# Optimization experiments

Measured on AMD Instinct MI355X. Metric: run time of the kernel, lower is better.

Reference implementation:

```python
import jax, jax.numpy as jnp
import numpy as np

OLD = (32, 32)   # fine grid coord_dims
NEW = (16, 16)   # coarse grid (dims // 2)
N_ORDERS = 6     # multi-indices of total order <= 2 in 2 coords


def lin_resize(x, new_size, axis):
    # 1D linear interpolation along `axis`, align_corners=True (matches F.interpolate)
    old = x.shape[axis]
    pos = jnp.arange(new_size, dtype=x.dtype) * ((old - 1) / (new_size - 1))
    lo = jnp.clip(jnp.floor(pos).astype(jnp.int32), 0, old - 2)
    w = pos - lo.astype(x.dtype)
    xl = jnp.take(x, lo, axis=axis)
    xh = jnp.take(x, lo + 1, axis=axis)
    shp = [1] * x.ndim
    shp[axis] = new_size
    w = w.reshape(shp)
    return xl * (1.0 - w) + xh * w


def bilinear_resize(x, new_hw):
    # separable bilinear, align_corners=True; x is [..., H, W]
    x = lin_resize(x, new_hw[0], x.ndim - 2)
    return lin_resize(x, new_hw[1], x.ndim - 1)


def setup_inputs():
    key = jax.random.key(0)
    ks = jax.random.split(key, 6)
    B = 32                      # bs * n_ind_dim = 8 * 4
    G = OLD[0] * OLD[1]         # fine grid size = 1024
    m, n = 2048, 1536           # coarse constraints x coarse vars (16*16*6)
    return {
        "coeffs": jax.random.normal(ks[0], (B, G, N_ORDERS), jnp.float32),
        "rhs": jax.random.normal(ks[1], (B, G), jnp.float32),
        "steps_x": jax.random.uniform(ks[2], (B, OLD[0] - 1), jnp.float32),
        "steps_y": jax.random.uniform(ks[3], (B, OLD[1] - 1), jnp.float32),
        "A": jax.random.normal(ks[4], (B, m, n), jnp.float32) * 0.05,
        "A_rhs": jax.random.normal(ks[5], (B, m), jnp.float32),
    }


def reference(coeffs, rhs, steps_x, steps_y, A, A_rhs):
    B = coeffs.shape[0]
    new_G = NEW[0] * NEW[1]

    # --- downsample_coeffs: [B,G,O] -> [B,O,H,W] -> bilinear -> [B,newG,O]
    c = coeffs.transpose(0, 2, 1).reshape(B, N_ORDERS, OLD[0], OLD[1])
    c = bilinear_resize(c, NEW)
    new_coeffs = c.reshape(B, N_ORDERS, new_G).transpose(0, 2, 1)

    # --- downsample_rhs: [B,G] -> [B,1,H,W] -> bilinear -> [B,newG]
    r = bilinear_resize(rhs.reshape(B, 1, OLD[0], OLD[1]), NEW)
    new_rhs = r.reshape(B, new_G)

    # --- downsample_steps: drop last, pairwise sum
    nsx = steps_x[:, :-1].reshape(B, OLD[0] // 2 - 1, 2).sum(axis=-1)
    nsy = steps_y[:, :-1].reshape(B, OLD[1] // 2 - 1, 2).sum(axis=-1)

    # --- make_AtA (coarsest path: dense bmm) ---
    AtA = jnp.einsum('bmn,bmk->bnk', A, A)           # At @ A, [B,n,n]
    AtPrhs = jnp.einsum('bmn,bm->bn', A, A_rhs)      # At @ rhs
    D = jnp.sum(A * A, axis=1)                       # diag(AtA) = column sums of squares

    # --- L/U split (get_tril): L = cols <= rows, U = cols > rows ---
    n = AtA.shape[-1]
    ridx = jnp.arange(n)
    lmask = ridx[:, None] >= ridx[None, :]
    L = jnp.where(lmask, AtA, jnp.zeros((), AtA.dtype))
    U = jnp.where(lmask, jnp.zeros((), AtA.dtype), AtA)

    return (new_coeffs, new_rhs, nsx, nsy, AtA, AtPrhs, D, L, U)
```

## Files before the change

### kernel.cpp

```cpp
#include <hip/hip_runtime.h>
#include <math.h>

#define NB 32
#define M 2048
#define N 1536
#define NORD 6

#define OFF_COEFFS 0
#define OFF_RHS    49152
#define OFF_NSX    57344
#define OFF_NSY    57824
#define OFF_ATA    58304
#define OFF_ATPRHS 75555776
#define OFF_D      75604928
#define OFF_L      75654080
#define OFF_U      151151552
#define SMALL_TOTAL 58304

typedef short short8v __attribute__((ext_vector_type(8)));
typedef float f32x4 __attribute__((ext_vector_type(4)));

__device__ __forceinline__ void gload16(const void* g, void* l) {
    __builtin_amdgcn_global_load_lds(
        (const __attribute__((address_space(1))) void*)g,
        (__attribute__((address_space(3))) void*)l, 16, 0, 0);
}

__device__ __forceinline__ uint rtn_bf16(float x) {
    uint u = __float_as_uint(x);
    return (u + 0x7fffu + ((u >> 16) & 1u)) >> 16;
}

__device__ __forceinline__ void nts(float v, float* p) {
    __builtin_nontemporal_store(v, p);
}
__device__ __forceinline__ void nts4(f32x4 v, float* p) {
    __builtin_nontemporal_store(v, (f32x4*)p);
}

__global__ void small_kernel(const float* __restrict__ coeffs,
                             const float* __restrict__ rhs,
                             const float* __restrict__ sx,
                             const float* __restrict__ sy,
                             float* __restrict__ out) {
    int idx = blockIdx.x * blockDim.x + threadIdx.x;
    if (idx >= SMALL_TOTAL) return;
    const float scale = 31.0f / 15.0f;
    if (idx < 49152) {
        int b = idx / 1536;
        int rem = idx % 1536;
        int gp = rem / 6;
        int o  = rem % 6;
        int yy = gp / 16, xx = gp % 16;
        float py = (float)yy * scale;
        int ly = (int)floorf(py); if (ly > 30) ly = 30;
        float wy = py - (float)ly;
        float px = (float)xx * scale;
        int lx = (int)floorf(px); if (lx > 30) lx = 30;
        float wx = px - (float)lx;
        const float* base = coeffs + (size_t)b * 1024 * NORD;
        float v00 = base[(ly * 32 + lx) * NORD + o];
        float v01 = base[(ly * 32 + lx + 1) * NORD + o];
        float v10 = base[((ly + 1) * 32 + lx) * NORD + o];
        float v11 = base[((ly + 1) * 32 + lx + 1) * NORD + o];
        float a  = v00 * (1.0f - wy) + v10 * wy;
        float bb = v01 * (1.0f - wy) + v11 * wy;
        out[OFF_COEFFS + idx] = a * (1.0f - wx) + bb * wx;
    } else if (idx < 57344) {
        int j = idx - 49152;
        int b = j / 256;
        int gp = j % 256;
        int yy = gp / 16, xx = gp % 16;
        float py = (float)yy * scale;
        int ly = (int)floorf(py); if (ly > 30) ly = 30;
        float wy = py - (float)ly;
        float px = (float)xx * scale;
        int lx = (int)floorf(px); if (lx > 30) lx = 30;
        float wx = px - (float)lx;
        const float* base = rhs + (size_t)b * 1024;
        float v00 = base[ly * 32 + lx];
        float v01 = base[ly * 32 + lx + 1];
        float v10 = base[(ly + 1) * 32 + lx];
        float v11 = base[(ly + 1) * 32 + lx + 1];
        float a  = v00 * (1.0f - wy) + v10 * wy;
        float bb = v01 * (1.0f - wy) + v11 * wy;
        out[OFF_RHS + j] = a * (1.0f - wx) + bb * wx;
    } else if (idx < 57824) {
        int j = idx - 57344;
        int b = j / 15, k = j % 15;
        out[OFF_NSX + j] = sx[b * 31 + 2 * k] + sx[b * 31 + 2 * k + 1];
    } else {
        int j = idx - 57824;
        int b = j / 15, k = j % 15;
        out[OFF_NSY + j] = sy[b * 31 + 2 * k] + sy[b * 31 + 2 * k + 1];
    }
}

__global__ __launch_bounds__(256) void split_kernel(const float* __restrict__ A,
                                                    const float* __restrict__ Arhs,
                                                    ushort* __restrict__ Ahi,
                                                    float2* __restrict__ part) {
    int bid = blockIdx.x;
    int q  = bid & 3;
    int cb = (bid >> 2) % 6;
    int b  = bid / 24;
    int t  = threadIdx.x;
    int col = cb * 256 + t;
    const float* Ab = A + (size_t)b * M * N;
    const float* rb = Arhs + (size_t)b * M;
    uint4* Hp = (uint4*)Ahi;
    float s1 = 0.0f, s2 = 0.0f;
    for (int oct = q * 64; oct < q * 64 + 64; ++oct) {
        uint hw[4];
#pragma unroll
        for (int j = 0; j < 4; ++j) {
            float a0 = Ab[(size_t)(oct * 8 + 2 * j) * N + col];
            float a1 = Ab[(size_t)(oct * 8 + 2 * j + 1) * N + col];
            float r0 = rb[oct * 8 + 2 * j];
            float r1 = rb[oct * 8 + 2 * j + 1];
            s1 = fmaf(a0, r0, s1); s1 = fmaf(a1, r1, s1);
            s2 = fmaf(a0, a0, s2); s2 = fmaf(a1, a1, s2);
            hw[j] = rtn_bf16(a0) | (rtn_bf16(a1) << 16);
        }
        Hp[(size_t)(b * 256 + oct) * N + col] = make_uint4(hw[0], hw[1], hw[2], hw[3]);
    }
    part[(size_t)q * (NB * 6 * 256) + (size_t)(b * 6 + cb) * 256 + t] = make_float2(s1, s2);
}

__global__ __launch_bounds__(256) void reduce_kernel(const float2* __restrict__ part,
                                                     float* __restrict__ out) {
    int idx = blockIdx.x * 256 + threadIdx.x;
    float s1 = 0.0f, s2 = 0.0f;
#pragma unroll
    for (int q = 0; q < 4; ++q) {
        float2 p = part[(size_t)q * (NB * 6 * 256) + idx];
        s1 += p.x; s2 += p.y;
    }
    out[OFF_ATPRHS + idx] = s1;
    out[OFF_D + idx] = s2;
}

#define SYRK_BLOCKS (NB * 42)

__global__ __launch_bounds__(512, 4) void syrk1_kernel(const ushort* __restrict__ Ahi,
                                                       float* __restrict__ out) {
    __shared__ ushort lds[3][1536 * 8];

    int bid = blockIdx.x;
    int swz = (bid % 8) * (SYRK_BLOCKS / 8) + bid / 8;
    int b  = swz / 42;
    int p2 = swz % 42;
    int p = p2 >> 1, half = p2 & 1;
    int ti = 0;
    while ((ti + 1) * (ti + 2) / 2 <= p) ++ti;
    int tj = p - ti * (ti + 1) / 2;
    bool diag = (ti == tj);
    int i0 = ti * 256;
    int j0 = tj * 256 + half * 128;

    int t = threadIdx.x, w = t >> 6, l = t & 63;
    int wr = w >> 1, wc = w & 1;
    int lc = l & 15, lg = l >> 4;

    const ushort* base = Ahi + (size_t)b * 256 * N * 8;

    f32x4 acc[4][4];
#pragma unroll
    for (int i = 0; i < 4; ++i)
#pragma unroll
        for (int j = 0; j < 4; ++j)
#pragma unroll
            for (int k = 0; k < 4; ++k) acc[i][j][k] = 0.0f;

    auto stage = [&](int buf, int s) {
        ushort* Lb = lds[buf];
#pragma unroll
        for (int q = 0; q < 2; ++q) {
            int g0 = q * 512 + w * 64;
            int oct = (g0 >> 8) & 3, col0 = g0 & 255;
            gload16(base + ((size_t)(s * 4 + oct) * N + i0 + col0 + l) * 8,
                    &Lb[(oct * 256 + col0) * 8]);
        }
        {
            int oct = w >> 1, col0 = (w & 1) * 64;
            gload16(base + ((size_t)(s * 4 + oct) * N + j0 + col0 + l) * 8,
                    &Lb[1024 * 8 + (oct * 128 + col0) * 8]);
        }
    };

    int cur = 0, stg = 2;
    stage(0, 0);
    stage(1, 1);

    for (int s = 0; s < 64; ++s) {
        if (s < 62) {
            stage(stg, s + 2);
            asm volatile("s_waitcnt vmcnt(6)" ::: "memory");
        } else if (s == 62) {
            asm volatile("s_waitcnt vmcnt(3)" ::: "memory");
        } else {
            asm volatile("s_waitcnt vmcnt(0)" ::: "memory");
        }
        __builtin_amdgcn_s_barrier();
        asm volatile("" ::: "memory");

        const ushort* Lc = lds[cur];
        short8v Bv[4];
#pragma unroll
        for (int bj = 0; bj < 4; ++bj) {
            int cp = wc * 64 + bj * 16 + lc;
            Bv[bj] = *(const short8v*)&Lc[1024 * 8 + (lg * 128 + cp) * 8];
        }
        __builtin_amdgcn_s_setprio(1);
#pragma unroll
        for (int ai = 0; ai < 4; ++ai) {
            short8v Av = *(const short8v*)&Lc[(lg * 256 + wr * 64 + ai * 16 + lc) * 8];
#pragma unroll
            for (int bj = 0; bj < 4; ++bj)
                acc[ai][bj] = __builtin_amdgcn_mfma_f32_16x16x32_bf16(Av, Bv[bj], acc[ai][bj], 0, 0, 0);
        }
        __builtin_amdgcn_s_setprio(0);

        asm volatile("" ::: "memory");
        __builtin_amdgcn_s_barrier();
        cur = (cur + 1 == 3) ? 0 : cur + 1;
        stg = (stg + 1 == 3) ? 0 : stg + 1;
    }

    float* AtA = out + OFF_ATA + (size_t)b * N * N;
    float* Lo  = out + OFF_L   + (size_t)b * N * N;
    float* Up  = out + OFF_U   + (size_t)b * N * N;

#pragma unroll
    for (int ai = 0; ai < 4; ++ai) {
        int gi0 = i0 + wr * 64 + ai * 16 + lg * 4;
#pragma unroll
        for (int bj = 0; bj < 4; ++bj) {
            int gj = j0 + wc * 64 + bj * 16 + lc;
#pragma unroll
            for (int r = 0; r < 4; ++r) {
                int gi = gi0 + r;
                float v = acc[ai][bj][r];
                size_t o = (size_t)gi * N + gj;
                nts(v, AtA + o);
                nts((gj <= gi) ? v : 0.0f, Lo + o);
                nts((gj >  gi) ? v : 0.0f, Up + o);
            }
            if (!diag) {
                f32x4 va = acc[ai][bj], vl, vu;
#pragma unroll
                for (int r = 0; r < 4; ++r) {
                    int gi = gi0 + r;
                    vl[r] = (gi <= gj) ? va[r] : 0.0f;
                    vu[r] = (gi >  gj) ? va[r] : 0.0f;
                }
                size_t om = (size_t)gj * N + gi0;
                nts4(va, AtA + om);
                nts4(vl, Lo  + om);
                nts4(vu, Up  + om);
            }
        }
    }
}

__global__ __launch_bounds__(256) void atp_d_kernel(const float* __restrict__ A,
                                                    const float* __restrict__ Arhs,
                                                    float* __restrict__ out) {
    int b  = blockIdx.x / 6;
    int cb = blockIdx.x % 6;
    int col = cb * 256 + threadIdx.x;
    const float* Ab = A + (size_t)b * M * N;
    const float* rb = Arhs + (size_t)b * M;
    float s1 = 0.0f, s2 = 0.0f;
#pragma unroll 4
    for (int m = 0; m < M; ++m) {
        float a = Ab[(size_t)m * N + col];
        float r = rb[m];
        s1 = fmaf(a, r, s1);
        s2 = fmaf(a, a, s2);
    }
    out[OFF_ATPRHS + b * N + col] = s1;
    out[OFF_D      + b * N + col] = s2;
}

#define BM 128
#define BK 16
#define NPAIRS 78

__global__ __launch_bounds__(256, 2) void syrk_kernel(const float* __restrict__ A,
                                                      float* __restrict__ out) {
    __shared__ float As[BK][BM];
    __shared__ float Bs[BK][BM];

    int bid = blockIdx.x;
    int b = bid / NPAIRS;
    int p = bid % NPAIRS;
    int ti = (int)((sqrtf(8.0f * (float)p + 1.0f) - 1.0f) * 0.5f);
    while ((ti + 1) * (ti + 2) / 2 <= p) ++ti;
    while (ti * (ti + 1) / 2 > p) --ti;
    int tj = p - ti * (ti + 1) / 2;
    int i0 = ti * BM, j0 = tj * BM;

    const float* Ab = A + (size_t)b * M * N;
    int t = threadIdx.x;
    int tx = t % 16, ty = t / 16;
    int lcv = (t % 32) * 4;
    int lk = t / 32;

    float acc[2][4][2][4] = {};

    for (int m0 = 0; m0 < M; m0 += BK) {
        const float* pa = Ab + (size_t)(m0 + lk) * N;
        float4 a0 = *(const float4*)(pa + i0 + lcv);
        float4 a1 = *(const float4*)(pa + (size_t)8 * N + i0 + lcv);
        float4 b0 = *(const float4*)(pa + j0 + lcv);
        float4 b1 = *(const float4*)(pa + (size_t)8 * N + j0 + lcv);
        *(float4*)&As[lk][lcv]     = a0;
        *(float4*)&As[lk + 8][lcv] = a1;
        *(float4*)&Bs[lk][lcv]     = b0;
        *(float4*)&Bs[lk + 8][lcv] = b1;
        __syncthreads();
#pragma unroll
        for (int kk = 0; kk < BK; ++kk) {
            float ar[2][4], br[2][4];
            *(float4*)&ar[0][0] = *(const float4*)&As[kk][ty * 4];
            *(float4*)&ar[1][0] = *(const float4*)&As[kk][64 + ty * 4];
            *(float4*)&br[0][0] = *(const float4*)&Bs[kk][tx * 4];
            *(float4*)&br[1][0] = *(const float4*)&Bs[kk][64 + tx * 4];
#pragma unroll
            for (int rh = 0; rh < 2; ++rh)
#pragma unroll
                for (int r = 0; r < 4; ++r)
#pragma unroll
                    for (int ch = 0; ch < 2; ++ch)
#pragma unroll
                        for (int c = 0; c < 4; ++c)
                            acc[rh][r][ch][c] = fmaf(ar[rh][r], br[ch][c], acc[rh][r][ch][c]);
        }
        __syncthreads();
    }

    float* AtA = out + OFF_ATA + (size_t)b * N * N;
    float* L   = out + OFF_L   + (size_t)b * N * N;
    float* U   = out + OFF_U   + (size_t)b * N * N;

#pragma unroll
    for (int rh = 0; rh < 2; ++rh)
#pragma unroll
        for (int r = 0; r < 4; ++r) {
            int gi = i0 + rh * 64 + ty * 4 + r;
#pragma unroll
            for (int ch = 0; ch < 2; ++ch) {
                int gjb = j0 + ch * 64 + tx * 4;
                float ta[4], tl[4], tu[4];
#pragma unroll
                for (int c = 0; c < 4; ++c) {
                    int gj = gjb + c;
                    float v = acc[rh][r][ch][c];
                    ta[c] = v;
                    tl[c] = (gj <= gi) ? v : 0.0f;
                    tu[c] = (gj >  gi) ? v : 0.0f;
                }
                size_t o = (size_t)gi * N + gjb;
                *(float4*)(AtA + o) = *(float4*)ta;
                *(float4*)(L   + o) = *(float4*)tl;
                *(float4*)(U   + o) = *(float4*)tu;
            }
        }

    if (ti != tj) {
#pragma unroll
        for (int ch = 0; ch < 2; ++ch)
#pragma unroll
            for (int c = 0; c < 4; ++c) {
                int gj = j0 + ch * 64 + tx * 4 + c;
#pragma unroll
                for (int rh = 0; rh < 2; ++rh) {
                    int gib = i0 + rh * 64 + ty * 4;
                    float ta[4], tl[4], tu[4];
#pragma unroll
                    for (int r = 0; r < 4; ++r) {
                        int gi = gib + r;
                        float v = acc[rh][r][ch][c];
                        ta[r] = v;
                        tl[r] = (gi <= gj) ? v : 0.0f;
                        tu[r] = (gi >  gj) ? v : 0.0f;
                    }
                    size_t o = (size_t)gj * N + gib;
                    *(float4*)(AtA + o) = *(float4*)ta;
                    *(float4*)(L   + o) = *(float4*)tl;
                    *(float4*)(U   + o) = *(float4*)tu;
                }
            }
    }
}

extern "C" void kernel_launch(void* const* d_in, const int* in_sizes, int n_in,
                              void* d_out, int out_size, void* d_ws, size_t ws_size,
                              hipStream_t stream) {
    const float* coeffs = (const float*)d_in[0];
    const float* rhs    = (const float*)d_in[1];
    const float* sx     = (const float*)d_in[2];
    const float* sy     = (const float*)d_in[3];
    const float* A      = (const float*)d_in[4];
    const float* Arhs   = (const float*)d_in[5];
    float* out = (float*)d_out;

    small_kernel<<<(SMALL_TOTAL + 255) / 256, 256, 0, stream>>>(coeffs, rhs, sx, sy, out);

    const size_t hi_bytes   = (size_t)NB * M * N * sizeof(ushort);
    const size_t part_bytes = (size_t)4 * NB * 6 * 256 * sizeof(float2);
    if (ws_size >= hi_bytes + part_bytes) {
        ushort* Ahi  = (ushort*)d_ws;
        float2* part = (float2*)((char*)d_ws + hi_bytes);
        split_kernel<<<768, 256, 0, stream>>>(A, Arhs, Ahi, part);
        reduce_kernel<<<192, 256, 0, stream>>>(part, out);
        syrk1_kernel<<<SYRK_BLOCKS, 512, 0, stream>>>(Ahi, out);
    } else {
        atp_d_kernel<<<NB * 6, 256, 0, stream>>>(A, Arhs, out);
        syrk_kernel<<<NB * NPAIRS, 256, 0, stream>>>(A, out);
    }
}
```

Baseline: 515.0 us.

## Use full 256x256 SYRK tiles with 32x32x16 MFMA and shared diagonal panel

The SYRK kernel now computes a full 256x256 output tile per block instead of splitting it into two 256x128 halves. It uses 32x32x16 bf16 MFMA instructions, and diagonal tiles load a single panel that serves as both A and B. The goal is to raise arithmetic intensity, halve the redundant panel loads, and cut the number of LDS reads per MFMA. In exchange the block uses more LDS (three 32KB buffers) and more accumulator registers, which drops occupancy to 2 blocks per CU and leaves fewer blocks (672) in the grid.

```diff
diff --git a/kernel.cpp b/kernel.cpp
--- a/kernel.cpp
+++ b/kernel.cpp
@@ -19,6 +19,7 @@
 
 typedef short short8v __attribute__((ext_vector_type(8)));
 typedef float f32x4 __attribute__((ext_vector_type(4)));
+typedef float f32x16 __attribute__((ext_vector_type(16)));
 
 __device__ __forceinline__ void gload16(const void* g, void* l) {
     __builtin_amdgcn_global_load_lds(
@@ -140,51 +141,55 @@
     out[OFF_D + idx] = s2;
 }
 
-#define SYRK_BLOCKS (NB * 42)
-
-__global__ __launch_bounds__(512, 4) void syrk1_kernel(const ushort* __restrict__ Ahi,
+#define SYRK2_BLOCKS (NB * 21)
+
+__global__ __launch_bounds__(512, 2) void syrk2_kernel(const ushort* __restrict__ Ahi,
                                                        float* __restrict__ out) {
-    __shared__ ushort lds[3][1536 * 8];
+    __shared__ ushort lds[3][2048 * 8];
 
     int bid = blockIdx.x;
-    int swz = (bid % 8) * (SYRK_BLOCKS / 8) + bid / 8;
-    int b  = swz / 42;
-    int p2 = swz % 42;
-    int p = p2 >> 1, half = p2 & 1;
+    int swz = (bid % 8) * (SYRK2_BLOCKS / 8) + bid / 8;
+    int b = swz / 21;
+    int p = swz % 21;
     int ti = 0;
     while ((ti + 1) * (ti + 2) / 2 <= p) ++ti;
     int tj = p - ti * (ti + 1) / 2;
     bool diag = (ti == tj);
-    int i0 = ti * 256;
-    int j0 = tj * 256 + half * 128;
+    int i0 = ti * 256, j0 = tj * 256;
 
     int t = threadIdx.x, w = t >> 6, l = t & 63;
     int wr = w >> 1, wc = w & 1;
-    int lc = l & 15, lg = l >> 4;
+    int l31 = l & 31, hi = l >> 5;
 
     const ushort* base = Ahi + (size_t)b * 256 * N * 8;
 
-    f32x4 acc[4][4];
-#pragma unroll
-    for (int i = 0; i < 4; ++i)
+    f32x16 acc[2][4];
+#pragma unroll
+    for (int i = 0; i < 2; ++i)
 #pragma unroll
         for (int j = 0; j < 4; ++j)
 #pragma unroll
-            for (int k = 0; k < 4; ++k) acc[i][j][k] = 0.0f;
+            for (int k = 0; k < 16; ++k) acc[i][j][k] = 0.0f;
 
     auto stage = [&](int buf, int s) {
         ushort* Lb = lds[buf];
-#pragma unroll
-        for (int q = 0; q < 2; ++q) {
-            int g0 = q * 512 + w * 64;
-            int oct = (g0 >> 8) & 3, col0 = g0 & 255;
-            gload16(base + ((size_t)(s * 4 + oct) * N + i0 + col0 + l) * 8,
-                    &Lb[(oct * 256 + col0) * 8]);
-        }
-        {
-            int oct = w >> 1, col0 = (w & 1) * 64;
-            gload16(base + ((size_t)(s * 4 + oct) * N + j0 + col0 + l) * 8,
-                    &Lb[1024 * 8 + (oct * 128 + col0) * 8]);
+        if (!diag) {
+            int jw = w >> 2;
+            int cw = (w & 3) * 4;
+            const ushort* gb = base + ((size_t)s * 4 * N + (jw ? j0 : i0)) * 8;
+            ushort* pb = Lb + jw * (1024 * 8);
+#pragma unroll
+            for (int q = 0; q < 4; ++q) {
+                int c = cw + q, oct = c >> 2, col0 = (c & 3) * 64;
+                gload16(gb + ((size_t)oct * N + col0 + l) * 8, &pb[(oct * 256 + col0) * 8]);
+            }
+        } else {
+            const ushort* gb = base + ((size_t)s * 4 * N + i0) * 8;
+#pragma unroll
+            for (int q = 0; q < 2; ++q) {
+                int c = w * 2 + q, oct = c >> 2, col0 = (c & 3) * 64;
+                gload16(gb + ((size_t)oct * N + col0 + l) * 8, &Lb[(oct * 256 + col0) * 8]);
+            }
         }
     };
 
@@ -195,9 +200,11 @@
     for (int s = 0; s < 64; ++s) {
         if (s < 62) {
             stage(stg, s + 2);
-            asm volatile("s_waitcnt vmcnt(6)" ::: "memory");
+            if (diag) asm volatile("s_waitcnt vmcnt(4)" ::: "memory");
+            else      asm volatile("s_waitcnt vmcnt(8)" ::: "memory");
         } else if (s == 62) {
-            asm volatile("s_waitcnt vmcnt(3)" ::: "memory");
+            if (diag) asm volatile("s_waitcnt vmcnt(2)" ::: "memory");
+            else      asm volatile("s_waitcnt vmcnt(4)" ::: "memory");
         } else {
             asm volatile("s_waitcnt vmcnt(0)" ::: "memory");
         }
@@ -205,19 +212,22 @@
         asm volatile("" ::: "memory");
 
         const ushort* Lc = lds[cur];
-        short8v Bv[4];
-#pragma unroll
-        for (int bj = 0; bj < 4; ++bj) {
-            int cp = wc * 64 + bj * 16 + lc;
-            Bv[bj] = *(const short8v*)&Lc[1024 * 8 + (lg * 128 + cp) * 8];
-        }
+        const ushort* Bpan = Lc + (diag ? 0 : 1024 * 8);
         __builtin_amdgcn_s_setprio(1);
 #pragma unroll
-        for (int ai = 0; ai < 4; ++ai) {
-            short8v Av = *(const short8v*)&Lc[(lg * 256 + wr * 64 + ai * 16 + lc) * 8];
+        for (int ks = 0; ks < 2; ++ks) {
+            int octb = ks * 2 + hi;
+            short8v Bv[4];
 #pragma unroll
             for (int bj = 0; bj < 4; ++bj)
-                acc[ai][bj] = __builtin_amdgcn_mfma_f32_16x16x32_bf16(Av, Bv[bj], acc[ai][bj], 0, 0, 0);
+                Bv[bj] = *(const short8v*)&Bpan[((size_t)(octb * 256 + wc * 128 + bj * 32 + l31)) * 8];
+#pragma unroll
+            for (int ai = 0; ai < 2; ++ai) {
+                short8v Av = *(const short8v*)&Lc[((size_t)(octb * 256 + wr * 64 + ai * 32 + l31)) * 8];
+#pragma unroll
+                for (int bj = 0; bj < 4; ++bj)
+                    acc[ai][bj] = __builtin_amdgcn_mfma_f32_32x32x16_bf16(Av, Bv[bj], acc[ai][bj], 0, 0, 0);
+            }
         }
         __builtin_amdgcn_s_setprio(0);
 
@@ -232,32 +242,38 @@
     float* Up  = out + OFF_U   + (size_t)b * N * N;
 
 #pragma unroll
-    for (int ai = 0; ai < 4; ++ai) {
-        int gi0 = i0 + wr * 64 + ai * 16 + lg * 4;
+    for (int ai = 0; ai < 2; ++ai) {
+        int gi0 = i0 + wr * 64 + ai * 32 + 4 * hi;
 #pragma unroll
         for (int bj = 0; bj < 4; ++bj) {
-            int gj = j0 + wc * 64 + bj * 16 + lc;
-#pragma unroll
-            for (int r = 0; r < 4; ++r) {
-                int gi = gi0 + r;
-                float v = acc[ai][bj][r];
-                size_t o = (size_t)gi * N + gj;
-                nts(v, AtA + o);
-                nts((gj <= gi) ? v : 0.0f, Lo + o);
-                nts((gj >  gi) ? v : 0.0f, Up + o);
-            }
-            if (!diag) {
-                f32x4 va = acc[ai][bj], vl, vu;
-#pragma unroll
-                for (int r = 0; r < 4; ++r) {
-                    int gi = gi0 + r;
-                    vl[r] = (gi <= gj) ? va[r] : 0.0f;
-                    vu[r] = (gi >  gj) ? va[r] : 0.0f;
+            int gj = j0 + wc * 128 + bj * 32 + l31;
+#pragma unroll
+            for (int q = 0; q < 4; ++q) {
+#pragma unroll
+                for (int rr = 0; rr < 4; ++rr) {
+                    int gi = gi0 + 8 * q + rr;
+                    float v = acc[ai][bj][q * 4 + rr];
+                    size_t o = (size_t)gi * N + gj;
+                    nts(v, AtA + o);
+                    nts((gj <= gi) ? v : 0.0f, Lo + o);
+                    nts((gj >  gi) ? v : 0.0f, Up + o);
                 }
-                size_t om = (size_t)gj * N + gi0;
-                nts4(va, AtA + om);
-                nts4(vl, Lo  + om);
-                nts4(vu, Up  + om);
+                if (!diag) {
+                    int gib = gi0 + 8 * q;
+                    f32x4 va, vl, vu;
+#pragma unroll
+                    for (int rr = 0; rr < 4; ++rr) {
+                        int gi = gib + rr;
+                        float v = acc[ai][bj][q * 4 + rr];
+                        va[rr] = v;
+                        vl[rr] = (gi <= gj) ? v : 0.0f;
+                        vu[rr] = (gi >  gj) ? v : 0.0f;
+                    }
+                    size_t om = (size_t)gj * N + gib;
+                    nts4(va, AtA + om);
+                    nts4(vl, Lo  + om);
+                    nts4(vu, Up  + om);
+                }
             }
         }
     }
@@ -415,7 +431,7 @@
         float2* part = (float2*)((char*)d_ws + hi_bytes);
         split_kernel<<<768, 256, 0, stream>>>(A, Arhs, Ahi, part);
         reduce_kernel<<<192, 256, 0, stream>>>(part, out);
-        syrk1_kernel<<<SYRK_BLOCKS, 512, 0, stream>>>(Ahi, out);
+        syrk2_kernel<<<SYRK2_BLOCKS, 512, 0, stream>>>(Ahi, out);
     } else {
         atp_d_kernel<<<NB * 6, 256, 0, stream>>>(A, Arhs, out);
         syrk_kernel<<<NB * NPAIRS, 256, 0, stream>>>(A, out);
```

After: 855.7 us. 1.66x slower.

## Make SYRK kernel persistent with atomic tile counter scheduling

Applied to the files above, without the earlier changes.

Replaces the one-block-per-tile SYRK launch with 512 persistent blocks that fetch tile indices from a global atomic counter. The counter is reset by the preceding reduce kernel. This drops the XCD swizzle and aims to cut block launch overhead and tail imbalance. In exchange it adds an atomic and two barriers per tile and loses the L2-locality swizzle across XCDs.

```diff
diff --git a/kernel.cpp b/kernel.cpp
--- a/kernel.cpp
+++ b/kernel.cpp
@@ -128,7 +128,9 @@
 }
 
 __global__ __launch_bounds__(256) void reduce_kernel(const float2* __restrict__ part,
-                                                     float* __restrict__ out) {
+                                                     float* __restrict__ out,
+                                                     int* __restrict__ ctr) {
+    if (blockIdx.x == 0 && threadIdx.x == 0) *ctr = 0;
     int idx = blockIdx.x * 256 + threadIdx.x;
     float s1 = 0.0f, s2 = 0.0f;
 #pragma unroll
@@ -140,124 +142,133 @@
     out[OFF_D + idx] = s2;
 }
 
-#define SYRK_BLOCKS (NB * 42)
+#define SYRK_TILES (NB * 42)
+#define SYRK_PERSIST 512
 
 __global__ __launch_bounds__(512, 4) void syrk1_kernel(const ushort* __restrict__ Ahi,
-                                                       float* __restrict__ out) {
+                                                       float* __restrict__ out,
+                                                       int* __restrict__ ctr) {
     __shared__ ushort lds[3][1536 * 8];
-
-    int bid = blockIdx.x;
-    int swz = (bid % 8) * (SYRK_BLOCKS / 8) + bid / 8;
-    int b  = swz / 42;
-    int p2 = swz % 42;
-    int p = p2 >> 1, half = p2 & 1;
-    int ti = 0;
-    while ((ti + 1) * (ti + 2) / 2 <= p) ++ti;
-    int tj = p - ti * (ti + 1) / 2;
-    bool diag = (ti == tj);
-    int i0 = ti * 256;
-    int j0 = tj * 256 + half * 128;
+    __shared__ int tile_s;
 
     int t = threadIdx.x, w = t >> 6, l = t & 63;
     int wr = w >> 1, wc = w & 1;
     int lc = l & 15, lg = l >> 4;
 
-    const ushort* base = Ahi + (size_t)b * 256 * N * 8;
-
-    f32x4 acc[4][4];
-#pragma unroll
-    for (int i = 0; i < 4; ++i)
-#pragma unroll
-        for (int j = 0; j < 4; ++j)
-#pragma unroll
-            for (int k = 0; k < 4; ++k) acc[i][j][k] = 0.0f;
-
-    auto stage = [&](int buf, int s) {
-        ushort* Lb = lds[buf];
-#pragma unroll
-        for (int q = 0; q < 2; ++q) {
-            int g0 = q * 512 + w * 64;
-            int oct = (g0 >> 8) & 3, col0 = g0 & 255;
-            gload16(base + ((size_t)(s * 4 + oct) * N + i0 + col0 + l) * 8,
-                    &Lb[(oct * 256 + col0) * 8]);
+    for (;;) {
+        if (t == 0) tile_s = atomicAdd(ctr, 1);
+        __syncthreads();
+        int tile = tile_s;
+        __syncthreads();
+        if (tile >= SYRK_TILES) return;
+
+        int b  = tile / 42;
+        int p2 = tile % 42;
+        int p = p2 >> 1, half = p2 & 1;
+        int ti = 0;
+        while ((ti + 1) * (ti + 2) / 2 <= p) ++ti;
+        int tj = p - ti * (ti + 1) / 2;
+        bool diag = (ti == tj);
+        int i0 = ti * 256;
+        int j0 = tj * 256 + half * 128;
+
+        const ushort* base = Ahi + (size_t)b * 256 * N * 8;
+
+        f32x4 acc[4][4];
+#pragma unroll
+        for (int i = 0; i < 4; ++i)
+#pragma unroll
+            for (int j = 0; j < 4; ++j)
+#pragma unroll
+                for (int k = 0; k < 4; ++k) acc[i][j][k] = 0.0f;
+
+        auto stage = [&](int buf, int s) {
+            ushort* Lb = lds[buf];
+#pragma unroll
+            for (int q = 0; q < 2; ++q) {
+                int g0 = q * 512 + w * 64;
+                int oct = (g0 >> 8) & 3, col0 = g0 & 255;
+                gload16(base + ((size_t)(s * 4 + oct) * N + i0 + col0 + l) * 8,
+                        &Lb[(oct * 256 + col0) * 8]);
+            }
+            {
+                int oct = w >> 1, col0 = (w & 1) * 64;
+                gload16(base + ((size_t)(s * 4 + oct) * N + j0 + col0 + l) * 8,
+                        &Lb[1024 * 8 + (oct * 128 + col0) * 8]);
+            }
+        };
+
+        int cur = 0, stg = 2;
+        stage(0, 0);
+        stage(1, 1);
+
+        for (int s = 0; s < 64; ++s) {
+            if (s < 62) {
+                stage(stg, s + 2);
+                asm volatile("s_waitcnt vmcnt(6)" ::: "memory");
+            } else if (s == 62) {
+                asm volatile("s_waitcnt vmcnt(3)" ::: "memory");
+            } else {
+                asm volatile("s_waitcnt vmcnt(0)" ::: "memory");
+            }
+            __builtin_amdgcn_s_barrier();
+            asm volatile("" ::: "memory");
+
+            const ushort* Lc = lds[cur];
+            short8v Bv[4];
+#pragma unroll
+            for (int bj = 0; bj < 4; ++bj) {
+                int cp = wc * 64 + bj * 16 + lc;
+                Bv[bj] = *(const short8v*)&Lc[1024 * 8 + (lg * 128 + cp) * 8];
+            }
+            __builtin_amdgcn_s_setprio(1);
+#pragma unroll
+            for (int ai = 0; ai < 4; ++ai) {
+                short8v Av = *(const short8v*)&Lc[(lg * 256 + wr * 64 + ai * 16 + lc) * 8];
+#pragma unroll
+                for (int bj = 0; bj < 4; ++bj)
+                    acc[ai][bj] = __builtin_amdgcn_mfma_f32_16x16x32_bf16(Av, Bv[bj], acc[ai][bj], 0, 0, 0);
+            }
+            __builtin_amdgcn_s_setprio(0);
+
+            asm volatile("" ::: "memory");
+            __builtin_amdgcn_s_barrier();
+            cur = (cur + 1 == 3) ? 0 : cur + 1;
+            stg = (stg + 1 == 3) ? 0 : stg + 1;
         }
-        {
-            int oct = w >> 1, col0 = (w & 1) * 64;
-            gload16(base + ((size_t)(s * 4 + oct) * N + j0 + col0 + l) * 8,
-                    &Lb[1024 * 8 + (oct * 128 + col0) * 8]);
-        }
-    };
-
-    int cur = 0, stg = 2;
-    stage(0, 0);
-    stage(1, 1);
-
-    for (int s = 0; s < 64; ++s) {
-        if (s < 62) {
-            stage(stg, s + 2);
-            asm volatile("s_waitcnt vmcnt(6)" ::: "memory");
-        } else if (s == 62) {
-            asm volatile("s_waitcnt vmcnt(3)" ::: "memory");
-        } else {
-            asm volatile("s_waitcnt vmcnt(0)" ::: "memory");
-        }
-        __builtin_amdgcn_s_barrier();
-        asm volatile("" ::: "memory");
-
-        const ushort* Lc = lds[cur];
-        short8v Bv[4];
-#pragma unroll
-        for (int bj = 0; bj < 4; ++bj) {
-            int cp = wc * 64 + bj * 16 + lc;
-            Bv[bj] = *(const short8v*)&Lc[1024 * 8 + (lg * 128 + cp) * 8];
-        }
-        __builtin_amdgcn_s_setprio(1);
+
+        float* AtA = out + OFF_ATA + (size_t)b * N * N;
+        float* Lo  = out + OFF_L   + (size_t)b * N * N;
+        float* Up  = out + OFF_U   + (size_t)b * N * N;
+
 #pragma unroll
         for (int ai = 0; ai < 4; ++ai) {
-            short8v Av = *(const short8v*)&Lc[(lg * 256 + wr * 64 + ai * 16 + lc) * 8];
-#pragma unroll
-            for (int bj = 0; bj < 4; ++bj)
-                acc[ai][bj] = __builtin_amdgcn_mfma_f32_16x16x32_bf16(Av, Bv[bj], acc[ai][bj], 0, 0, 0);
-        }
-        __builtin_amdgcn_s_setprio(0);
-
-        asm volatile("" ::: "memory");
-        __builtin_amdgcn_s_barrier();
-        cur = (cur + 1 == 3) ? 0 : cur + 1;
-        stg = (stg + 1 == 3) ? 0 : stg + 1;
-    }
-
-    float* AtA = out + OFF_ATA + (size_t)b * N * N;
-    float* Lo  = out + OFF_L   + (size_t)b * N * N;
-    float* Up  = out + OFF_U   + (size_t)b * N * N;
-
-#pragma unroll
-    for (int ai = 0; ai < 4; ++ai) {
-        int gi0 = i0 + wr * 64 + ai * 16 + lg * 4;
-#pragma unroll
-        for (int bj = 0; bj < 4; ++bj) {
-            int gj = j0 + wc * 64 + bj * 16 + lc;
-#pragma unroll
-            for (int r = 0; r < 4; ++r) {
-                int gi = gi0 + r;
-                float v = acc[ai][bj][r];
-                size_t o = (size_t)gi * N + gj;
-                nts(v, AtA + o);
-                nts((gj <= gi) ? v : 0.0f, Lo + o);
-                nts((gj >  gi) ? v : 0.0f, Up + o);
-            }
-            if (!diag) {
-                f32x4 va = acc[ai][bj], vl, vu;
+            int gi0 = i0 + wr * 64 + ai * 16 + lg * 4;
+#pragma unroll
+            for (int bj = 0; bj < 4; ++bj) {
+                int gj = j0 + wc * 64 + bj * 16 + lc;
 #pragma unroll
                 for (int r = 0; r < 4; ++r) {
                     int gi = gi0 + r;
-                    vl[r] = (gi <= gj) ? va[r] : 0.0f;
-                    vu[r] = (gi >  gj) ? va[r] : 0.0f;
+                    float v = acc[ai][bj][r];
+                    size_t o = (size_t)gi * N + gj;
+                    nts(v, AtA + o);
+                    nts((gj <= gi) ? v : 0.0f, Lo + o);
+                    nts((gj >  gi) ? v : 0.0f, Up + o);
                 }
-                size_t om = (size_t)gj * N + gi0;
-                nts4(va, AtA + om);
-                nts4(vl, Lo  + om);
-                nts4(vu, Up  + om);
+                if (!diag) {
+                    f32x4 va = acc[ai][bj], vl, vu;
+#pragma unroll
+                    for (int r = 0; r < 4; ++r) {
+                        int gi = gi0 + r;
+                        vl[r] = (gi <= gj) ? va[r] : 0.0f;
+                        vu[r] = (gi >  gj) ? va[r] : 0.0f;
+                    }
+                    size_t om = (size_t)gj * N + gi0;
+                    nts4(va, AtA + om);
+                    nts4(vl, Lo  + om);
+                    nts4(vu, Up  + om);
+                }
             }
         }
     }
@@ -410,12 +421,13 @@
 
     const size_t hi_bytes   = (size_t)NB * M * N * sizeof(ushort);
     const size_t part_bytes = (size_t)4 * NB * 6 * 256 * sizeof(float2);
-    if (ws_size >= hi_bytes + part_bytes) {
+    if (ws_size >= hi_bytes + part_bytes + 256) {
         ushort* Ahi  = (ushort*)d_ws;
         float2* part = (float2*)((char*)d_ws + hi_bytes);
+        int*    ctr  = (int*)((char*)d_ws + hi_bytes + part_bytes);
         split_kernel<<<768, 256, 0, stream>>>(A, Arhs, Ahi, part);
-        reduce_kernel<<<192, 256, 0, stream>>>(part, out);
-        syrk1_kernel<<<SYRK_BLOCKS, 512, 0, stream>>>(Ahi, out);
+        reduce_kernel<<<192, 256, 0, stream>>>(part, out, ctr);
+        syrk1_kernel<<<SYRK_PERSIST, 512, 0, stream>>>(Ahi, out, ctr);
     } else {
         atp_d_kernel<<<NB * 6, 256, 0, stream>>>(A, Arhs, out);
         syrk_kernel<<<NB * NPAIRS, 256, 0, stream>>>(A, out);
```

New measurement: 589.0 us. +14.4%, slower.
